# Kernel tuning notes

Hardware: AMD Instinct MI355X
Metric: run time of the kernel (lower is better)

## Reference

```python
import jax, jax.numpy as jnp
import numpy as np

HIDDEN = 2048
HEADS = 16
HEAD_DIM = HIDDEN // HEADS


def setup_inputs() -> dict:
    key = jax.random.key(0)
    ks = jax.random.split(key, 5)
    scale = 1.0 / np.sqrt(HIDDEN)
    x = jax.random.normal(ks[0], (2, 2048, HIDDEN), dtype=jnp.float32)
    wq = jax.random.normal(ks[1], (HIDDEN, HIDDEN), dtype=jnp.float32) * scale
    wk = jax.random.normal(ks[2], (HIDDEN, HIDDEN), dtype=jnp.float32) * scale
    wv = jax.random.normal(ks[3], (HIDDEN, HIDDEN), dtype=jnp.float32) * scale
    wo = jax.random.normal(ks[4], (HIDDEN, HIDDEN), dtype=jnp.float32) * scale
    return {"x": x, "wq": wq, "wk": wk, "wv": wv, "wo": wo}


def reference(x, wq, wk, wv, wo):
    B, S, D = x.shape
    # nn.Linear(w, bias=False): y = x @ w.T
    q = (x @ wq.T).reshape(B, S, HEADS, HEAD_DIM)
    k = (x @ wk.T).reshape(B, S, HEADS, HEAD_DIM)
    v = (x @ wv.T).reshape(B, S, HEADS, HEAD_DIM)
    scores = jnp.einsum("bqhd,bkhd->bhqk", q, k) / jnp.sqrt(
        jnp.asarray(HEAD_DIM, dtype=x.dtype)
    )
    causal_mask = jnp.triu(jnp.ones((S, S), dtype=bool), k=1)
    scores = jnp.where(causal_mask, -jnp.inf, scores)
    attn = jax.nn.softmax(scores, axis=-1)
    out = jnp.einsum("bhqk,bkhd->bqhd", attn, v).reshape(B, S, D)
    return out @ wo.T
```

## Files before the change

kernel.cpp:

```cpp
#include <hip/hip_runtime.h>
#include <hip/hip_bf16.h>
#include <math.h>

typedef unsigned short u16;
typedef __attribute__((ext_vector_type(8))) short bf16x8;
typedef __attribute__((ext_vector_type(4))) float f32x4;

__device__ static inline u16 f2bf(float f) {
  unsigned u = __float_as_uint(f);
  u += 0x7fff + ((u >> 16) & 1);
  return (u16)(u >> 16);
}

__device__ static inline void gload_lds16(const void* g, void* l) {
  __builtin_amdgcn_global_load_lds(
      (const __attribute__((address_space(1))) unsigned int*)g,
      (__attribute__((address_space(3))) unsigned int*)l, 16, 0, 0);
}

__device__ static inline void store_out(u16* p, float v)   { *p = f2bf(v); }
__device__ static inline void store_out(float* p, float v) { *p = v; }

__global__ void cvt_f32_bf16(const float* __restrict__ src, u16* __restrict__ dst, int n) {
  int stride = gridDim.x * blockDim.x;
  for (int i = blockIdx.x * blockDim.x + threadIdx.x; i * 8 < n; i += stride) {
    const float4* s4 = (const float4*)(src + (size_t)i * 8);
    float4 a = s4[0], b = s4[1];
    u16 t[8] = { f2bf(a.x), f2bf(a.y), f2bf(a.z), f2bf(a.w),
                 f2bf(b.x), f2bf(b.y), f2bf(b.z), f2bf(b.w) };
    *(bf16x8*)(dst + (size_t)i * 8) = *(bf16x8*)t;
  }
}

template <typename OutT>
__global__ __launch_bounds__(256, 2)
void gemm_bt(const u16* __restrict__ A, const u16* __restrict__ Bm,
             OutT* __restrict__ C, int M, int N, int K) {
  __shared__ u16 As[128 * 32];
  __shared__ u16 Bs[128 * 32];
  const int tid = threadIdx.x;
  const int lane = tid & 63;
  const int w = tid >> 6, wr = w >> 1, wc = w & 1;
  const int g = lane >> 4, l16 = lane & 15;
  const int row0 = blockIdx.y * 128, col0 = blockIdx.x * 128;
  f32x4 acc[4][4] = {};

  for (int k0 = 0; k0 < K; k0 += 32) {
    __syncthreads();
#pragma unroll
    for (int i = 0; i < 2; ++i) {
      int idx = i * 256 + tid;
      int r = idx >> 2, c = (idx & 3) * 8;
      gload_lds16(A  + (size_t)(row0 + r) * K + k0 + c, As + idx * 8);
      gload_lds16(Bm + (size_t)(col0 + r) * K + k0 + c, Bs + idx * 8);
    }
    __syncthreads();
    bf16x8 af[4], bfr[4];
#pragma unroll
    for (int m2 = 0; m2 < 4; ++m2)
      af[m2] = *(const bf16x8*)(As + (wr * 64 + m2 * 16 + l16) * 32 + g * 8);
#pragma unroll
    for (int n2 = 0; n2 < 4; ++n2)
      bfr[n2] = *(const bf16x8*)(Bs + (wc * 64 + n2 * 16 + l16) * 32 + g * 8);
#pragma unroll
    for (int m2 = 0; m2 < 4; ++m2)
#pragma unroll
      for (int n2 = 0; n2 < 4; ++n2)
        acc[m2][n2] = __builtin_amdgcn_mfma_f32_16x16x32_bf16(af[m2], bfr[n2], acc[m2][n2], 0, 0, 0);
  }

#pragma unroll
  for (int m2 = 0; m2 < 4; ++m2)
#pragma unroll
    for (int n2 = 0; n2 < 4; ++n2) {
      int col = col0 + wc * 64 + n2 * 16 + l16;
#pragma unroll
      for (int r = 0; r < 4; ++r) {
        int row = row0 + wr * 64 + m2 * 16 + g * 4 + r;
        store_out(C + (size_t)row * N + col, acc[m2][n2][r]);
      }
    }
}

__global__ __launch_bounds__(256)
void transpose_v(const u16* __restrict__ QKV, u16* __restrict__ Vt) {
  __shared__ u16 t[64][72];
  const int tid = threadIdx.x;
  const int b = blockIdx.y >> 5;
  const int s0 = (blockIdx.y & 31) * 64;
  const int hd0 = blockIdx.x * 64;
  const int lr = tid >> 2, lc = (tid & 3) * 16;
  const u16* src = QKV + ((size_t)(b * 2048 + s0 + lr) * 6144 + 4096 + hd0 + lc);
  *(bf16x8*)&t[lr][lc]     = *(const bf16x8*)src;
  *(bf16x8*)&t[lr][lc + 8] = *(const bf16x8*)(src + 8);
  __syncthreads();
  u16 tmp[16];
#pragma unroll
  for (int j = 0; j < 16; ++j) tmp[j] = t[lc + j][lr];
  u16* dst = Vt + ((size_t)(b * 2048 + hd0 + lr) * 2048 + s0 + lc);
  *(bf16x8*)dst       = *(bf16x8*)tmp;
  *(bf16x8*)(dst + 8) = *(bf16x8*)(tmp + 8);
}

__global__ __launch_bounds__(256, 2)
void attn_fwd(const u16* __restrict__ QKV, const u16* __restrict__ Vt,
              u16* __restrict__ AO) {
  __shared__ u16 Ks[64 * 128];
  __shared__ u16 Vs[128 * 64];
  __shared__ u16 Ps[4][16 * 64];
  const int tid = threadIdx.x, lane = tid & 63, w = tid >> 6;
  const int g = lane >> 4, l16 = lane & 15;
  const int bh = blockIdx.y, b = bh >> 4, h = bh & 15;
  const int fold = blockIdx.x;

  for (int phase = 0; phase < 2; ++phase) {
    const int qt = phase == 0 ? fold : 31 - fold;
    const int q0 = qt * 64 + w * 16;

    bf16x8 qf[4];
    {
      const u16* qrow = QKV + ((size_t)(b * 2048 + q0 + l16) * 6144 + h * 128 + g * 8);
#pragma unroll
      for (int c = 0; c < 4; ++c) qf[c] = *(const bf16x8*)(qrow + c * 32);
    }
    f32x4 o[8] = {};
    float mrun[4] = {-INFINITY, -INFINITY, -INFINITY, -INFINITY};
    float lrun[4] = {0.f, 0.f, 0.f, 0.f};

    const int kv_last = qt * 64;
    for (int kv0 = 0; kv0 <= kv_last; kv0 += 64) {
      __syncthreads();
#pragma unroll
      for (int i = 0; i < 4; ++i) {
        int idx = i * 256 + tid;
        {
          int row = idx >> 4;
          int scolb = ((idx & 15) * 16) ^ ((row & 7) << 4);
          gload_lds16((const char*)QKV +
                          ((size_t)(b * 2048 + kv0 + row) * 6144 + 2048 + h * 128) * 2 + scolb,
                      (char*)Ks + idx * 16);
        }
        {
          int d = idx >> 3;
          int vcolb = ((idx & 7) * 16) ^ ((d & 7) << 4);
          gload_lds16((const char*)Vt + ((size_t)(bh * 128 + d) * 2048 + kv0) * 2 + vcolb,
                      (char*)Vs + idx * 16);
        }
      }
      __syncthreads();

      f32x4 s[4];
#pragma unroll
      for (int kb = 0; kb < 4; ++kb) {
        f32x4 a = {};
        int row = kb * 16 + l16;
        int swz = (row & 7) << 4;
#pragma unroll
        for (int c = 0; c < 4; ++c) {
          bf16x8 kf = *(const bf16x8*)((const char*)Ks + row * 256 + ((c * 64 + g * 16) ^ swz));
          a = __builtin_amdgcn_mfma_f32_16x16x32_bf16(qf[c], kf, a, 0, 0, 0);
        }
        s[kb] = a * 0.08838834764831845f;
      }
      if (kv0 == kv_last) {
#pragma unroll
        for (int kb = 0; kb < 4; ++kb)
#pragma unroll
          for (int r = 0; r < 4; ++r)
            if (kv0 + kb * 16 + l16 > q0 + g * 4 + r) s[kb][r] = -INFINITY;
      }

      float mnew[4], al[4], rs[4];
#pragma unroll
      for (int r = 0; r < 4; ++r) {
        float t = fmaxf(fmaxf(s[0][r], s[1][r]), fmaxf(s[2][r], s[3][r]));
        t = fmaxf(t, __shfl_xor(t, 1));
        t = fmaxf(t, __shfl_xor(t, 2));
        t = fmaxf(t, __shfl_xor(t, 4));
        t = fmaxf(t, __shfl_xor(t, 8));
        mnew[r] = fmaxf(mrun[r], t);
        al[r] = __expf(mrun[r] - mnew[r]);
        mrun[r] = mnew[r];
        rs[r] = 0.f;
      }
      {
        int prow = g * 4;
#pragma unroll
        for (int kb = 0; kb < 4; ++kb)
#pragma unroll
          for (int r = 0; r < 4; ++r) {
            float p = __expf(s[kb][r] - mnew[r]);
            rs[r] += p;
            int row = prow + r;
            int byteoff = (kb * 32 + l16 * 2) ^ ((row & 7) << 4);
            *(u16*)((char*)Ps[w] + row * 128 + byteoff) = f2bf(p);
          }
      }
#pragma unroll
      for (int r = 0; r < 4; ++r) {
        float t = rs[r];
        t += __shfl_xor(t, 1);
        t += __shfl_xor(t, 2);
        t += __shfl_xor(t, 4);
        t += __shfl_xor(t, 8);
        lrun[r] = lrun[r] * al[r] + t;
      }
#pragma unroll
      for (int db = 0; db < 8; ++db)
#pragma unroll
        for (int r = 0; r < 4; ++r) o[db][r] *= al[r];

      bf16x8 pa[2];
      {
        int swz = (l16 & 7) << 4;
#pragma unroll
        for (int ks = 0; ks < 2; ++ks)
          pa[ks] = *(const bf16x8*)((const char*)Ps[w] + l16 * 128 + ((ks * 64 + g * 16) ^ swz));
      }
#pragma unroll
      for (int db = 0; db < 8; ++db) {
        int row = db * 16 + l16;
        int swz = (row & 7) << 4;
#pragma unroll
        for (int ks = 0; ks < 2; ++ks) {
          bf16x8 vf = *(const bf16x8*)((const char*)Vs + row * 128 + ((ks * 64 + g * 16) ^ swz));
          o[db] = __builtin_amdgcn_mfma_f32_16x16x32_bf16(pa[ks], vf, o[db], 0, 0, 0);
        }
      }
    }

#pragma unroll
    for (int r = 0; r < 4; ++r) {
      float rl = 1.0f / lrun[r];
      int q = q0 + g * 4 + r;
#pragma unroll
      for (int db = 0; db < 8; ++db)
        AO[(size_t)(b * 2048 + q) * 2048 + h * 128 + db * 16 + l16] = f2bf(o[db][r] * rl);
    }
  }
}

extern "C" void kernel_launch(void* const* d_in, const int* in_sizes, int n_in,
                              void* d_out, int out_size, void* d_ws, size_t ws_size,
                              hipStream_t stream) {
  const float* x  = (const float*)d_in[0];
  const float* wq = (const float*)d_in[1];
  const float* wk = (const float*)d_in[2];
  const float* wv = (const float*)d_in[3];
  const float* wo = (const float*)d_in[4];
  float* out = (float*)d_out;

  char* ws = (char*)d_ws;
  u16* Xb   = (u16*)(ws);
  u16* Wqkv = (u16*)(ws + ((size_t)16 << 20));
  u16* Wob  = (u16*)(ws + ((size_t)40 << 20));
  u16* QKV  = (u16*)(ws + ((size_t)48 << 20));
  u16* Vt   = (u16*)(ws + ((size_t)96 << 20));
  u16* AO   = (u16*)(ws + ((size_t)112 << 20));

  auto cvt = [&](const float* s, u16* d, int n) {
    int blocks = (n / 8 + 255) / 256;
    if (blocks > 2048) blocks = 2048;
    cvt_f32_bf16<<<blocks, 256, 0, stream>>>(s, d, n);
  };
  cvt(x,  Xb,              2 * 2048 * 2048);
  cvt(wq, Wqkv,            2048 * 2048);
  cvt(wk, Wqkv + 4194304,  2048 * 2048);
  cvt(wv, Wqkv + 8388608,  2048 * 2048);
  cvt(wo, Wob,             2048 * 2048);

  gemm_bt<u16><<<dim3(48, 32), 256, 0, stream>>>(Xb, Wqkv, QKV, 4096, 6144, 2048);
  transpose_v<<<dim3(32, 64), 256, 0, stream>>>(QKV, Vt);
  attn_fwd<<<dim3(16, 32), 256, 0, stream>>>(QKV, Vt, AO);
  gemm_bt<float><<<dim3(16, 32), 256, 0, stream>>>(AO, Wob, out, 4096, 2048, 2048);
}
```

Before: 411.7 us.

## Add 256x256 double-buffered pipelined GEMM for fused QKV projection

Replaces the 128x128 QKV projection GEMM with a new 512-thread kernel using 256x256 tiles, K-step 64, and double-buffered LDS. Global-to-LDS loads are staged in halves interleaved with MFMA quadrants under explicit waitcnt and barriers, and blocks are remapped for L2 locality. This aims to raise arithmetic intensity and overlap memory with compute in the largest GEMM. The cost is 128KB of LDS per block (limiting occupancy) and fragile hand-scheduled synchronisation. The attention kernel only gets local variable renames.

```diff
diff --git a/kernel.cpp b/kernel.cpp
--- a/kernel.cpp
+++ b/kernel.cpp
@@ -30,6 +30,128 @@
                  f2bf(b.x), f2bf(b.y), f2bf(b.z), f2bf(b.w) };
     *(bf16x8*)(dst + (size_t)i * 8) = *(bf16x8*)t;
   }
+}
+
+__global__ __launch_bounds__(512, 2)
+void gemm_bt_256(const u16* __restrict__ A, const u16* __restrict__ Bm,
+                 u16* __restrict__ C, int M, int N, int K) {
+  __shared__ u16 Abuf[2][256 * 64];
+  __shared__ u16 Bbuf[2][256 * 64];
+  const int tid = threadIdx.x, lane = tid & 63, w = tid >> 6;
+  const int wm = w >> 2, wn = w & 3;
+  const int g = lane >> 4, l16 = lane & 15;
+
+  const int per = gridDim.x >> 3;
+  const int swz = ((int)blockIdx.x & 7) * per + ((int)blockIdx.x >> 3);
+  const int nx = N >> 8;
+  const int bx = swz % nx, by = swz / nx;
+  const int brow = by << 8, bcol = bx << 8;
+  const int nt = K >> 6;
+
+  auto stage_half = [&](int sel, int kt, int d) {
+    const u16* src = (sel < 2) ? A : Bm;
+    const int rbase = (sel < 2) ? brow : bcol;
+    const int h = sel & 1;
+    char* lds = (char*)((sel < 2) ? Abuf[d] : Bbuf[d]) + h * 16384;
+#pragma unroll
+    for (int i = 0; i < 2; ++i) {
+      int idx = i * 512 + tid;
+      int r = h * 128 + (idx >> 3);
+      int c = ((idx & 7) * 16) ^ ((r & 7) << 4);
+      gload_lds16((const char*)(src + (size_t)(rbase + r) * K + kt * 64) + c,
+                  lds + idx * 16);
+    }
+  };
+
+  f32x4 acc[8][4] = {};
+  bf16x8 afr[4][2], bfr0[2][2], bfr1[2][2];
+
+  auto lda = [&](int d, int mf0) {
+#pragma unroll
+    for (int mf = 0; mf < 4; ++mf) {
+      int r = wm * 128 + (mf0 + mf) * 16 + l16;
+      const char* base = (const char*)Abuf[d] + r * 128;
+      int sw = (r & 7) << 4;
+#pragma unroll
+      for (int ks = 0; ks < 2; ++ks)
+        afr[mf][ks] = *(const bf16x8*)(base + ((ks * 64 + g * 16) ^ sw));
+    }
+  };
+  auto ldb = [&](int d, int nf0, bf16x8 bf[2][2]) {
+#pragma unroll
+    for (int nf = 0; nf < 2; ++nf) {
+      int r = wn * 64 + (nf0 + nf) * 16 + l16;
+      const char* base = (const char*)Bbuf[d] + r * 128;
+      int sw = (r & 7) << 4;
+#pragma unroll
+      for (int ks = 0; ks < 2; ++ks)
+        bf[nf][ks] = *(const bf16x8*)(base + ((ks * 64 + g * 16) ^ sw));
+    }
+  };
+
+#define WAIT_LGKM() do { \
+    asm volatile("s_waitcnt lgkmcnt(0)" ::: "memory"); \
+    __builtin_amdgcn_sched_barrier(0); } while (0)
+#define QUAD(MF0, NF0, BFR) do { \
+    __builtin_amdgcn_s_setprio(1); \
+    _Pragma("unroll") for (int mf = 0; mf < 4; ++mf) \
+    _Pragma("unroll") for (int nf = 0; nf < 2; ++nf) \
+    _Pragma("unroll") for (int ks = 0; ks < 2; ++ks) \
+      acc[MF0 + mf][NF0 + nf] = __builtin_amdgcn_mfma_f32_16x16x32_bf16( \
+          afr[mf][ks], BFR[nf][ks], acc[MF0 + mf][NF0 + nf], 0, 0, 0); \
+    __builtin_amdgcn_s_setprio(0); } while (0)
+
+  stage_half(0, 0, 0); stage_half(1, 0, 0);
+  stage_half(2, 0, 0); stage_half(3, 0, 0);
+  stage_half(2, 1, 1); stage_half(3, 1, 1);
+  asm volatile("s_waitcnt vmcnt(4)" ::: "memory");
+  __builtin_amdgcn_sched_barrier(0);
+  __builtin_amdgcn_s_barrier();
+
+  for (int t = 0; t < nt; ++t) {
+    const int cur = t & 1;
+    lda(cur, 0); ldb(cur, 0, bfr0);
+    if (t + 1 < nt) stage_half(0, t + 1, cur ^ 1);
+    __builtin_amdgcn_s_barrier();
+    WAIT_LGKM();
+    QUAD(0, 0, bfr0);
+    __builtin_amdgcn_s_barrier();
+    ldb(cur, 2, bfr1);
+    if (t + 1 < nt) stage_half(1, t + 1, cur ^ 1);
+    __builtin_amdgcn_s_barrier();
+    WAIT_LGKM();
+    QUAD(0, 2, bfr1);
+    __builtin_amdgcn_s_barrier();
+    lda(cur, 4);
+    if (t + 2 < nt) stage_half(2, t + 2, cur);
+    __builtin_amdgcn_s_barrier();
+    WAIT_LGKM();
+    QUAD(4, 2, bfr1);
+    __builtin_amdgcn_s_barrier();
+    if (t + 2 < nt) stage_half(3, t + 2, cur);
+    QUAD(4, 0, bfr0);
+    if (t + 1 < nt) {
+      if (t + 2 < nt) asm volatile("s_waitcnt vmcnt(4)" ::: "memory");
+      else            asm volatile("s_waitcnt vmcnt(0)" ::: "memory");
+      __builtin_amdgcn_sched_barrier(0);
+      __builtin_amdgcn_s_barrier();
+    }
+  }
+#undef WAIT_LGKM
+#undef QUAD
+
+  const size_t cb = (size_t)(brow + wm * 128) * N + bcol + wn * 64;
+#pragma unroll
+  for (int mf = 0; mf < 8; ++mf)
+#pragma unroll
+    for (int nf = 0; nf < 4; ++nf) {
+      int col = nf * 16 + l16;
+#pragma unroll
+      for (int rr = 0; rr < 4; ++rr) {
+        int row = mf * 16 + g * 4 + rr;
+        C[cb + (size_t)row * N + col] = f2bf(acc[mf][nf][rr]);
+      }
+    }
 }
 
 template <typename OutT>
@@ -154,10 +276,10 @@
       for (int kb = 0; kb < 4; ++kb) {
         f32x4 a = {};
         int row = kb * 16 + l16;
-        int swz = (row & 7) << 4;
+        int swzk = (row & 7) << 4;
 #pragma unroll
         for (int c = 0; c < 4; ++c) {
-          bf16x8 kf = *(const bf16x8*)((const char*)Ks + row * 256 + ((c * 64 + g * 16) ^ swz));
+          bf16x8 kf = *(const bf16x8*)((const char*)Ks + row * 256 + ((c * 64 + g * 16) ^ swzk));
           a = __builtin_amdgcn_mfma_f32_16x16x32_bf16(qf[c], kf, a, 0, 0, 0);
         }
         s[kb] = a * 0.08838834764831845f;
@@ -212,18 +334,18 @@
 
       bf16x8 pa[2];
       {
-        int swz = (l16 & 7) << 4;
+        int swzp = (l16 & 7) << 4;
 #pragma unroll
         for (int ks = 0; ks < 2; ++ks)
-          pa[ks] = *(const bf16x8*)((const char*)Ps[w] + l16 * 128 + ((ks * 64 + g * 16) ^ swz));
+          pa[ks] = *(const bf16x8*)((const char*)Ps[w] + l16 * 128 + ((ks * 64 + g * 16) ^ swzp));
       }
 #pragma unroll
       for (int db = 0; db < 8; ++db) {
         int row = db * 16 + l16;
-        int swz = (row & 7) << 4;
+        int swzv = (row & 7) << 4;
 #pragma unroll
         for (int ks = 0; ks < 2; ++ks) {
-          bf16x8 vf = *(const bf16x8*)((const char*)Vs + row * 128 + ((ks * 64 + g * 16) ^ swz));
+          bf16x8 vf = *(const bf16x8*)((const char*)Vs + row * 128 + ((ks * 64 + g * 16) ^ swzv));
           o[db] = __builtin_amdgcn_mfma_f32_16x16x32_bf16(pa[ks], vf, o[db], 0, 0, 0);
         }
       }
@@ -269,7 +391,7 @@
   cvt(wv, Wqkv + 8388608,  2048 * 2048);
   cvt(wo, Wob,             2048 * 2048);
 
-  gemm_bt<u16><<<dim3(48, 32), 256, 0, stream>>>(Xb, Wqkv, QKV, 4096, 6144, 2048);
+  gemm_bt_256<<<384, 512, 0, stream>>>(Xb, Wqkv, QKV, 4096, 6144, 2048);
   transpose_v<<<dim3(32, 64), 256, 0, stream>>>(QKV, Vt);
   attn_fwd<<<dim3(16, 32), 256, 0, stream>>>(QKV, Vt, AO);
   gemm_bt<float><<<dim3(16, 32), 256, 0, stream>>>(AO, Wob, out, 4096, 2048, 2048);
```

After: 413.6 us. About the same (+0.4%).
